# Kernel optimization log

Measured on AMD Instinct MI355X. Metric: run time of the kernel, lower is better.

## Reference

```python
import jax, jax.numpy as jnp
import numpy as np

SIGMA = 4.0
KSIZE = 2 * int(4.0 * SIGMA + 0.5) + 1  # 33, as in AnomalyMapGenerator
IMAGE_SIZE = (224, 224)


def _gaussian_kernel1d(ksize, sigma):
    x = jnp.arange(ksize, dtype=jnp.float32) - ksize // 2
    g = jnp.exp(-(x * x) / (2.0 * sigma * sigma))
    return g / jnp.sum(g)


def _gaussian_blur2d(x):
    # x: [B, 1, H, W]; kornia-style GaussianBlur2d with reflect padding
    g = _gaussian_kernel1d(KSIZE, SIGMA)
    k2 = jnp.outer(g, g)[None, None]  # [1,1,K,K]
    pad = KSIZE // 2
    xp = jnp.pad(x, ((0, 0), (0, 0), (pad, pad), (pad, pad)), mode='reflect')
    return jax.lax.conv_general_dilated(xp, k2, (1, 1), 'VALID')


def _cdist(a, b):
    # Euclidean distance matrix [Na, Nb] via the expanded quadratic form
    d2 = (jnp.sum(a * a, axis=1)[:, None]
          + jnp.sum(b * b, axis=1)[None, :]
          - 2.0 * (a @ b.T))
    return jnp.sqrt(jnp.maximum(d2, 1e-12))


def setup_inputs() -> dict:
    key = jax.random.key(0)
    k1, k2 = jax.random.split(key)
    B, H, W, C, M = 16, 28, 28, 128, 16384
    embedding = jax.random.normal(k1, (B * H * W, C), dtype=jnp.float32)
    memory_bank = jax.random.normal(k2, (M, C), dtype=jnp.float32)
    return {
        'embedding': embedding,
        'memory_bank': memory_bank,
        'batch_size': B,
        'width': W,
        'height': H,
        'num_neighbors': 9,
    }


def reference(embedding, memory_bank, batch_size, width, height, num_neighbors):
    N, C = embedding.shape
    # 1-NN search: [N, M] distance matrix
    dists = _cdist(embedding, memory_bank)
    locations_flat = jnp.argmin(dists, axis=1)                      # [N]
    patch_scores_flat = jnp.take_along_axis(
        dists, locations_flat[:, None], axis=1)[:, 0]                # [N]
    patch_scores = patch_scores_flat.reshape(batch_size, -1)        # [B, HW]
    locations = locations_flat.reshape(batch_size, -1)              # [B, HW]

    # compute_anomaly_score (softmax-reweighted max patch score)
    brange = jnp.arange(batch_size)
    max_patches = jnp.argmax(patch_scores, axis=1)                  # [B]
    score = patch_scores[brange, max_patches]                       # s* per image
    nn_index = locations[brange, max_patches]                       # [B]
    nn_sample = memory_bank[nn_index]                               # [B, C]
    d_nn = _cdist(nn_sample, memory_bank)                           # [B, M]
    _, support = jax.lax.top_k(-d_nn, num_neighbors)                # [B, k]
    max_feats = embedding.reshape(batch_size, -1, C)[brange, max_patches]  # [B, C]
    support_feats = memory_bank[support]                            # [B, k, C]
    d = jnp.sqrt(jnp.maximum(
        jnp.sum((max_feats[:, None, :] - support_feats) ** 2, axis=-1), 1e-12))  # [B, k]
    weights = 1.0 - jax.nn.softmax(d, axis=1)[:, 0]
    pred_score = weights * score                                    # [B]

    # anomaly map: nearest interpolate [B,1,w,h] -> IMAGE_SIZE, then blur
    pmap = patch_scores.reshape(batch_size, 1, width, height)
    rows = jnp.arange(IMAGE_SIZE[0]) * width // IMAGE_SIZE[0]
    cols = jnp.arange(IMAGE_SIZE[1]) * height // IMAGE_SIZE[1]
    up = pmap[:, :, rows][:, :, :, cols]                            # [B,1,224,224]
    anomaly_map = _gaussian_blur2d(up)
    return anomaly_map, pred_score
```

## Files before the change

### kernel.cpp

```cpp
#include <hip/hip_runtime.h>
#include <math.h>

#define C 128
#define BIAS 256.0f

typedef __attribute__((ext_vector_type(8))) short short8;
typedef __attribute__((ext_vector_type(4))) float f32x4;
typedef __attribute__((ext_vector_type(4))) unsigned int uint4v;
typedef unsigned short u16;
typedef unsigned int u32;
typedef unsigned long long u64;

static __device__ __forceinline__ u16 f2bf(float f) {
  unsigned int u = __builtin_bit_cast(unsigned int, f);
  unsigned int r = (u + 0x7fffu + ((u >> 16) & 1u)) >> 16;
  return (u16)r;
}

static __device__ __forceinline__ float bf2f(short s) {
  return __uint_as_float(((u32)(u16)s) << 16);
}

static __device__ __forceinline__ void gload_lds16(const void* g, void* l) {
  __builtin_amdgcn_global_load_lds(
      (const __attribute__((address_space(1))) unsigned int*)g,
      (__attribute__((address_space(3))) unsigned int*)l, 16, 0, 0);
}

__global__ __launch_bounds__(256) void prep_kernel(
    const float* __restrict__ emb, const float* __restrict__ bank,
    u16* __restrict__ Abf, u16* __restrict__ Bbf, float* __restrict__ anorm,
    float* __restrict__ bnorm, u64* __restrict__ packed, int N, int M) {
  const int tid = threadIdx.x;
  const int chunk = blockIdx.x * 256 + tid;
  const int total = (N + M) * (C / 8);
  if (chunk >= total) return;
  if (chunk < N) packed[chunk] = ~0ull;
  const int gr = chunk >> 4;
  const int co = (chunk & 15) * 8;
  const float* src;
  u16* dst;
  float* ndst;
  int r;
  float sc;
  if (gr < N) { src = emb; dst = Abf; ndst = anorm; r = gr; sc = 1.0f; }
  else { src = bank; dst = Bbf; ndst = bnorm; r = gr - N; sc = -2.0f; }
  const float* p = src + (size_t)r * C + co;
  float4 v0 = *(const float4*)p;
  float4 v1 = *(const float4*)(p + 4);
  u16 o[8] = {f2bf(sc * v0.x), f2bf(sc * v0.y), f2bf(sc * v0.z),
              f2bf(sc * v0.w), f2bf(sc * v1.x), f2bf(sc * v1.y),
              f2bf(sc * v1.z), f2bf(sc * v1.w)};
  *(uint4v*)(dst + (size_t)r * C + co) = *(const uint4v*)o;
  float s = v0.x * v0.x + v0.y * v0.y + v0.z * v0.z + v0.w * v0.w +
            v1.x * v1.x + v1.y * v1.y + v1.z * v1.z + v1.w * v1.w;
#pragma unroll
  for (int m = 1; m <= 8; m <<= 1) s += __shfl_xor(s, m, 64);
  if ((tid & 15) == 0) ndst[r] = s;
}

__global__ __launch_bounds__(256, 4) void nn_mfma(
    const u16* __restrict__ Abf, const u16* __restrict__ Bbf,
    const float* __restrict__ bnorm, const float* __restrict__ anorm,
    u64* __restrict__ packed, int N, int M) {
  __shared__ short Bs[2][8192];
  const int tid = threadIdx.x;
  const int lane = tid & 63;
  const int w = tid >> 6;
  const int lr = lane & 15, kg = lane >> 4;
  const int bid = blockIdx.x;
  const int sub = bid & 15;
  const int row0 = (bid >> 4) * 128;
  const int j0base = (sub & 7) * (M >> 3) + (sub >> 3) * (M >> 4);

  int soff[4];
#pragma unroll
  for (int q = 0; q < 4; ++q) {
    const int r = q * 16 + (tid >> 4);
    const int c = (((tid & 15) * 16) ^ ((r & 7) << 4)) >> 1;
    soff[q] = r * C + c;
  }

#define STAGE(bufi, jj)                                                     \
  do {                                                                      \
    const u16* gsrc = Bbf + (size_t)(jj) * C;                               \
    _Pragma("unroll") for (int q = 0; q < 4; ++q)                           \
        gload_lds16(gsrc + soff[q], &Bs[bufi][q * 2048 + w * 512]);         \
  } while (0)

  short8 af[2][4];
  {
    const u16* pa = Abf + (size_t)(row0 + w * 32 + lr) * C + kg * 8;
#pragma unroll
    for (int fi = 0; fi < 2; ++fi)
#pragma unroll
      for (int k = 0; k < 4; ++k)
        af[fi][k] = *(const short8*)(pa + fi * 16 * C + k * 32);
  }

  u32 minv[8];
#pragma unroll
  for (int s = 0; s < 8; ++s) minv[s] = 0xFFFFFFFFu;

  STAGE(0, j0base);

  const float* bnp = bnorm + j0base + lr;
  float bnc[4], bnn[4];
#pragma unroll
  for (int fj = 0; fj < 4; ++fj) bnc[fj] = bnp[fj * 16] + BIAS;

  __syncthreads();

  int j0 = j0base;
  for (int t = 0; t < 16; ++t) {
    const int buf = t & 1;
    if (t < 15) {
      STAGE(buf ^ 1, j0 + 64);
#pragma unroll
      for (int fj = 0; fj < 4; ++fj)
        bnn[fj] = bnp[(t + 1) * 64 + fj * 16] + BIAS;
    }

    f32x4 acc[2][4];
#pragma unroll
    for (int fi = 0; fi < 2; ++fi)
#pragma unroll
      for (int fj = 0; fj < 4; ++fj)
        acc[fi][fj] = (f32x4){bnc[fj], bnc[fj], bnc[fj], bnc[fj]};

    const short* bsb = &Bs[buf][0];
    const int cxor = (lr & 7) << 3;
#pragma unroll
    for (int k = 0; k < 4; ++k) {
      const int ko = (k * 32 + kg * 8) ^ cxor;
      short8 bf[4];
#pragma unroll
      for (int fj = 0; fj < 4; ++fj)
        bf[fj] = *(const short8*)&bsb[(fj * 16 + lr) * C + ko];
#pragma unroll
      for (int fi = 0; fi < 2; ++fi)
#pragma unroll
        for (int fj = 0; fj < 4; ++fj)
          acc[fi][fj] = __builtin_amdgcn_mfma_f32_16x16x32_bf16(
              af[fi][k], bf[fj], acc[fi][fj], 0, 0, 0);
    }

#pragma unroll
    for (int fj = 0; fj < 4; ++fj) {
      const u32 col = (u32)(j0 + fj * 16 + lr);
#pragma unroll
      for (int fi = 0; fi < 2; ++fi) {
#pragma unroll
        for (int r = 0; r < 4; ++r) {
          u32 key = (__float_as_uint(acc[fi][fj][r]) & 0xFFFFC000u) | col;
          const int s = fi * 4 + r;
          minv[s] = key < minv[s] ? key : minv[s];
        }
      }
    }
#pragma unroll
    for (int fj = 0; fj < 4; ++fj) bnc[fj] = bnn[fj];
    __syncthreads();
    j0 += 64;
  }
#undef STAGE

#pragma unroll
  for (int s = 0; s < 8; ++s) {
    u32 k = minv[s];
#pragma unroll
    for (int m = 1; m <= 8; m <<= 1) {
      u32 ok = (u32)__shfl_xor((int)k, m, 64);
      k = ok < k ? ok : k;
    }
    if (lr == 0) {
      const int row = row0 + w * 32 + (s >> 2) * 16 + kg * 4 + (s & 3);
      const u32 col = k & 0x3FFFu;
      const float vm = __uint_as_float(k & 0xFFFFC000u);
      float d2 = fmaxf(anorm[row] + (vm - BIAS), 0.0f);
      u64 pk = ((u64)__float_as_uint(d2) << 32) | col;
      atomicMin(&packed[row], pk);
    }
  }
}

__global__ __launch_bounds__(256) void rescore_part(
    const u16* __restrict__ Bbf, const float* __restrict__ bnorm,
    const u64* __restrict__ packed, float* __restrict__ score,
    int* __restrict__ maxrow, float* __restrict__ cvals,
    int* __restrict__ cidx, int M) {
  const int c = blockIdx.x;
  const int b = blockIdx.y;
  const int tid = threadIdx.x;
  __shared__ float vecf[C];
  __shared__ float sv[256];
  __shared__ int si[256];
  __shared__ int sl[256];

  {
    float bv = -INFINITY;
    int bi_ = 0x7fffffff, bl = 0;
    for (int i = tid; i < 784; i += 256) {
      u64 p = packed[(size_t)b * 784 + i];
      float v = __uint_as_float((unsigned)(p >> 32));
      if (v > bv) { bv = v; bi_ = i; bl = (int)(unsigned)p; }
    }
    sv[tid] = bv; si[tid] = bi_; sl[tid] = bl;
    __syncthreads();
    for (int s = 128; s > 0; s >>= 1) {
      if (tid < s) {
        if (sv[tid + s] > sv[tid] ||
            (sv[tid + s] == sv[tid] && si[tid + s] < si[tid])) {
          sv[tid] = sv[tid + s]; si[tid] = si[tid + s]; sl[tid] = sl[tid + s];
        }
      }
      __syncthreads();
    }
  }
  const int nn = sl[0];
  if (c == 0 && tid == 0) {
    score[b] = sqrtf(fmaxf(sv[0], 1e-12f));
    maxrow[b] = b * 784 + si[0];
  }
  __syncthreads();

  if (tid < 16) {
    short8 v = ((const short8*)(Bbf + (size_t)nn * C))[tid];
#pragma unroll
    for (int e = 0; e < 8; ++e) vecf[tid * 8 + e] = bf2f(v[e]);
  }
  __syncthreads();
  const float nnorm = bnorm[nn];
  const int j0 = c * (M >> 4);
  float rv[4];
  int rj[4];
#pragma unroll
  for (int q = 0; q < 4; ++q) {
    const int j = j0 + q * 256 + tid;
    const short8* br = (const short8*)(Bbf + (size_t)j * C);
    float dot = 0.0f;
#pragma unroll
    for (int kc = 0; kc < 16; ++kc) {
      short8 v = br[kc];
      float4 w0 = *(const float4*)&vecf[kc * 8];
      float4 w1 = *(const float4*)&vecf[kc * 8 + 4];
      dot += bf2f(v[0]) * w0.x + bf2f(v[1]) * w0.y + bf2f(v[2]) * w0.z +
             bf2f(v[3]) * w0.w + bf2f(v[4]) * w1.x + bf2f(v[5]) * w1.y +
             bf2f(v[6]) * w1.z + bf2f(v[7]) * w1.w;
    }
    rv[q] = nnorm + bnorm[j] - 0.5f * dot;
    rj[q] = j;
  }
  for (int s9 = 0; s9 < 9; ++s9) {
    float bv = INFINITY;
    int bj = 0x7fffffff;
#pragma unroll
    for (int q = 0; q < 4; ++q)
      if (rv[q] < bv) { bv = rv[q]; bj = rj[q]; }
    sv[tid] = bv; si[tid] = bj;
    __syncthreads();
    for (int s = 128; s > 0; s >>= 1) {
      if (tid < s) {
        if (sv[tid + s] < sv[tid] ||
            (sv[tid + s] == sv[tid] && si[tid + s] < si[tid])) {
          sv[tid] = sv[tid + s]; si[tid] = si[tid + s];
        }
      }
      __syncthreads();
    }
    const int selj = si[0];
    if (tid == 0) {
      cvals[((size_t)b * 16 + c) * 9 + s9] = sv[0];
      cidx[((size_t)b * 16 + c) * 9 + s9] = selj;
    }
#pragma unroll
    for (int q = 0; q < 4; ++q)
      if (rj[q] == selj) rv[q] = INFINITY;
    __syncthreads();
  }
}

__global__ __launch_bounds__(256) void rescore_merge(
    const float* __restrict__ emb, const float* __restrict__ Bk,
    const float* __restrict__ cvals, const int* __restrict__ cidx,
    const float* __restrict__ score, const int* __restrict__ maxrow,
    float* __restrict__ pred) {
  const int b = blockIdx.x;
  const int tid = threadIdx.x;
  const int w = tid >> 6, lane = tid & 63;
  __shared__ float wv[144];
  __shared__ int wi[144];
  __shared__ float sv[256];
  __shared__ int si[256];
  __shared__ int sp[256];
  __shared__ int sup[9];
  __shared__ float vec[C];
  __shared__ float ds[9];
  if (tid < 144) {
    wv[tid] = cvals[(size_t)b * 144 + tid];
    wi[tid] = cidx[(size_t)b * 144 + tid];
  }
  if (tid < 32)
    *(float4*)&vec[tid * 4] =
        *(const float4*)(emb + (size_t)maxrow[b] * C + tid * 4);
  __syncthreads();
  for (int s9 = 0; s9 < 9; ++s9) {
    if (tid < 144) { sv[tid] = wv[tid]; si[tid] = wi[tid]; sp[tid] = tid; }
    else { sv[tid] = INFINITY; si[tid] = 0x7fffffff; sp[tid] = -1; }
    __syncthreads();
    for (int s = 128; s > 0; s >>= 1) {
      if (tid < s) {
        if (sv[tid + s] < sv[tid] ||
            (sv[tid + s] == sv[tid] && si[tid + s] < si[tid])) {
          sv[tid] = sv[tid + s]; si[tid] = si[tid + s]; sp[tid] = sp[tid + s];
        }
      }
      __syncthreads();
    }
    if (tid == 0) {
      sup[s9] = si[0];
      wv[sp[0]] = INFINITY;
    }
    __syncthreads();
  }
  for (int s = w; s < 9; s += 4) {
    const float* br = Bk + (size_t)sup[s] * C;
    float d0 = vec[lane * 2] - br[lane * 2];
    float d1 = vec[lane * 2 + 1] - br[lane * 2 + 1];
    float acc = d0 * d0 + d1 * d1;
#pragma unroll
    for (int m = 1; m <= 32; m <<= 1) acc += __shfl_xor(acc, m, 64);
    if (lane == 0) ds[s] = sqrtf(fmaxf(acc, 1e-12f));
  }
  __syncthreads();
  if (tid == 0) {
    float m = ds[0];
    for (int t = 1; t < 9; ++t) m = fmaxf(m, ds[t]);
    float sum = 0.0f, e0 = 0.0f;
    for (int t = 0; t < 9; ++t) {
      float e = expf(ds[t] - m);
      sum += e;
      if (t == 0) e0 = e;
    }
    pred[b] = (1.0f - e0 / sum) * score[b];
  }
}

__global__ __launch_bounds__(256) void blur_fused(
    const u64* __restrict__ packed, float* __restrict__ out) {
  const int y = blockIdx.x, b = blockIdx.y;
  const int tid = threadIdx.x;
  __shared__ float g[33];
  __shared__ float rows[6][28];
  if (tid < 33) {
    float d = (float)tid - 16.0f;
    g[tid] = expf(-(d * d) * (1.0f / 32.0f));
  }
  int rcmin = 27;
  for (int t = 0; t < 33; ++t) {
    int yy = y + t - 16;
    yy = yy < 0 ? -yy : (yy > 223 ? 446 - yy : yy);
    int rc = yy >> 3;
    rcmin = rc < rcmin ? rc : rcmin;
  }
  if (tid < 168) {
    const int i = tid / 28, cc = tid - i * 28;
    int rc = rcmin + i;
    rc = rc > 27 ? 27 : rc;
    u64 p = packed[(size_t)b * 784 + rc * 28 + cc];
    float d2 = __uint_as_float((unsigned)(p >> 32));
    rows[i][cc] = sqrtf(fmaxf(d2, 1e-12f));
  }
  __syncthreads();
  float gv[6];
#pragma unroll
  for (int i = 0; i < 6; ++i) gv[i] = 0.0f;
  for (int t = 0; t < 33; ++t) {
    int yy = y + t - 16;
    yy = yy < 0 ? -yy : (yy > 223 ? 446 - yy : yy);
    const int idx = (yy >> 3) - rcmin;
    const float gt = g[t];
#pragma unroll
    for (int i = 0; i < 6; ++i) gv[i] += (idx == i) ? gt : 0.0f;
  }
  if (tid < 224) {
    float hacc[6];
#pragma unroll
    for (int i = 0; i < 6; ++i) hacc[i] = 0.0f;
    for (int s = 0; s < 33; ++s) {
      int xx = tid + s - 16;
      xx = xx < 0 ? -xx : (xx > 223 ? 446 - xx : xx);
      const int cs = xx >> 3;
      const float gs_ = g[s];
#pragma unroll
      for (int i = 0; i < 6; ++i) hacc[i] += gs_ * rows[i][cs];
    }
    float acc = 0.0f, gsum = 0.0f;
#pragma unroll
    for (int i = 0; i < 6; ++i) { acc += gv[i] * hacc[i]; gsum += gv[i]; }
    out[((size_t)b * 224 + y) * 224 + tid] = acc / (gsum * gsum);
  }
}

extern "C" void kernel_launch(void* const* d_in, const int* in_sizes, int n_in,
                              void* d_out, int out_size, void* d_ws,
                              size_t ws_size, hipStream_t stream) {
  const float* emb = (const float*)d_in[0];
  const float* bank = (const float*)d_in[1];
  const int N = in_sizes[0] / C;
  const int M = in_sizes[1] / C;
  const int B = 16;

  u16* Abf = (u16*)d_ws;
  u16* Bbf = Abf + (size_t)N * C;
  u64* packed = (u64*)(Bbf + (size_t)M * C);
  float* anorm = (float*)(packed + N);
  float* bnorm = anorm + N;
  float* score = bnorm + M;
  int* maxrow = (int*)(score + B);
  float* cvals = (float*)(maxrow + B);
  int* cidx = (int*)(cvals + B * 144);

  float* out_map = (float*)d_out;
  float* out_pred = out_map + (size_t)B * 224 * 224;

  const int total = (N + M) * (C / 8);
  prep_kernel<<<(total + 255) / 256, 256, 0, stream>>>(emb, bank, Abf, Bbf,
                                                       anorm, bnorm, packed,
                                                       N, M);
  nn_mfma<<<(N / 128) * 16, 256, 0, stream>>>(Abf, Bbf, bnorm, anorm, packed,
                                              N, M);
  blur_fused<<<dim3(224, B), 256, 0, stream>>>(packed, out_map);
  rescore_part<<<dim3(16, B), 256, 0, stream>>>(Bbf, bnorm, packed, score,
                                                maxrow, cvals, cidx, M);
  rescore_merge<<<B, 256, 0, stream>>>(emb, bank, cvals, cidx, score, maxrow,
                                       out_pred);
}
```

Before: 139.3 us.

## Fuse rescore merge via last-block atomic counter and batch blur rows per block

The separate rescore merge kernel is folded into the partial rescore kernel. A per-image atomic counter lets the last of 32 blocks perform the final top-9 merge and softmax weighting. The partial search is split across twice as many blocks, each covering half as many bank rows, to raise parallelism. The blur kernel now computes 8 output rows per block, sharing one horizontal pass over 5 source rows, and hoists the normalization into a single reciprocal. Together these aim to cut launch overhead and redundant horizontal blur work, at the cost of threadfence and atomic synchronization and more candidates in the merge.

```diff
diff --git a/kernel.cpp b/kernel.cpp
--- a/kernel.cpp
+++ b/kernel.cpp
@@ -30,12 +30,14 @@
 __global__ __launch_bounds__(256) void prep_kernel(
     const float* __restrict__ emb, const float* __restrict__ bank,
     u16* __restrict__ Abf, u16* __restrict__ Bbf, float* __restrict__ anorm,
-    float* __restrict__ bnorm, u64* __restrict__ packed, int N, int M) {
+    float* __restrict__ bnorm, u64* __restrict__ packed, int* __restrict__ cnt,
+    int N, int M) {
   const int tid = threadIdx.x;
   const int chunk = blockIdx.x * 256 + tid;
   const int total = (N + M) * (C / 8);
   if (chunk >= total) return;
   if (chunk < N) packed[chunk] = ~0ull;
+  if (chunk < 16) cnt[chunk] = 0;
   const int gr = chunk >> 4;
   const int co = (chunk & 15) * 8;
   const float* src;
@@ -184,11 +186,13 @@
   }
 }
 
-__global__ __launch_bounds__(256) void rescore_part(
+__global__ __launch_bounds__(256) void rescore_fused(
     const u16* __restrict__ Bbf, const float* __restrict__ bnorm,
-    const u64* __restrict__ packed, float* __restrict__ score,
+    const u64* __restrict__ packed, const float* __restrict__ emb,
+    const float* __restrict__ Bk, float* __restrict__ score,
     int* __restrict__ maxrow, float* __restrict__ cvals,
-    int* __restrict__ cidx, int M) {
+    int* __restrict__ cidx, int* __restrict__ cnt, float* __restrict__ pred,
+    int M) {
   const int c = blockIdx.x;
   const int b = blockIdx.y;
   const int tid = threadIdx.x;
@@ -196,6 +200,11 @@
   __shared__ float sv[256];
   __shared__ int si[256];
   __shared__ int sl[256];
+  __shared__ float wv[288];
+  __shared__ int wi[288];
+  __shared__ int sp[256];
+  __shared__ int sup[9];
+  __shared__ float ds[9];
 
   {
     float bv = -INFINITY;
@@ -231,11 +240,11 @@
   }
   __syncthreads();
   const float nnorm = bnorm[nn];
-  const int j0 = c * (M >> 4);
-  float rv[4];
-  int rj[4];
-#pragma unroll
-  for (int q = 0; q < 4; ++q) {
+  const int j0 = c * (M >> 5);
+  float rv[2];
+  int rj[2];
+#pragma unroll
+  for (int q = 0; q < 2; ++q) {
     const int j = j0 + q * 256 + tid;
     const short8* br = (const short8*)(Bbf + (size_t)j * C);
     float dot = 0.0f;
@@ -255,7 +264,7 @@
     float bv = INFINITY;
     int bj = 0x7fffffff;
 #pragma unroll
-    for (int q = 0; q < 4; ++q)
+    for (int q = 0; q < 2; ++q)
       if (rv[q] < bv) { bv = rv[q]; bj = rj[q]; }
     sv[tid] = bv; si[tid] = bj;
     __syncthreads();
@@ -270,43 +279,40 @@
     }
     const int selj = si[0];
     if (tid == 0) {
-      cvals[((size_t)b * 16 + c) * 9 + s9] = sv[0];
-      cidx[((size_t)b * 16 + c) * 9 + s9] = selj;
-    }
-#pragma unroll
-    for (int q = 0; q < 4; ++q)
+      cvals[((size_t)b * 32 + c) * 9 + s9] = sv[0];
+      cidx[((size_t)b * 32 + c) * 9 + s9] = selj;
+    }
+#pragma unroll
+    for (int q = 0; q < 2; ++q)
       if (rj[q] == selj) rv[q] = INFINITY;
     __syncthreads();
   }
-}
-
-__global__ __launch_bounds__(256) void rescore_merge(
-    const float* __restrict__ emb, const float* __restrict__ Bk,
-    const float* __restrict__ cvals, const int* __restrict__ cidx,
-    const float* __restrict__ score, const int* __restrict__ maxrow,
-    float* __restrict__ pred) {
-  const int b = blockIdx.x;
-  const int tid = threadIdx.x;
-  const int w = tid >> 6, lane = tid & 63;
-  __shared__ float wv[144];
-  __shared__ int wi[144];
-  __shared__ float sv[256];
-  __shared__ int si[256];
-  __shared__ int sp[256];
-  __shared__ int sup[9];
-  __shared__ float vec[C];
-  __shared__ float ds[9];
-  if (tid < 144) {
-    wv[tid] = cvals[(size_t)b * 144 + tid];
-    wi[tid] = cidx[(size_t)b * 144 + tid];
+
+  if (tid == 0) {
+    __threadfence();
+    sl[0] = atomicAdd(&cnt[b], 1);
+  }
+  __syncthreads();
+  if (sl[0] != 31) return;
+  __threadfence();
+
+  for (int i = tid; i < 288; i += 256) {
+    wv[i] = cvals[(size_t)b * 288 + i];
+    wi[i] = cidx[(size_t)b * 288 + i];
   }
   if (tid < 32)
-    *(float4*)&vec[tid * 4] =
+    *(float4*)&vecf[tid * 4] =
         *(const float4*)(emb + (size_t)maxrow[b] * C + tid * 4);
   __syncthreads();
   for (int s9 = 0; s9 < 9; ++s9) {
-    if (tid < 144) { sv[tid] = wv[tid]; si[tid] = wi[tid]; sp[tid] = tid; }
-    else { sv[tid] = INFINITY; si[tid] = 0x7fffffff; sp[tid] = -1; }
+    float bv = INFINITY;
+    int bi_ = 0x7fffffff, bp = -1;
+    for (int i = tid; i < 288; i += 256) {
+      if (wv[i] < bv || (wv[i] == bv && wi[i] < bi_)) {
+        bv = wv[i]; bi_ = wi[i]; bp = i;
+      }
+    }
+    sv[tid] = bv; si[tid] = bi_; sp[tid] = bp;
     __syncthreads();
     for (int s = 128; s > 0; s >>= 1) {
       if (tid < s) {
@@ -323,10 +329,11 @@
     }
     __syncthreads();
   }
+  const int w = tid >> 6, lane = tid & 63;
   for (int s = w; s < 9; s += 4) {
     const float* br = Bk + (size_t)sup[s] * C;
-    float d0 = vec[lane * 2] - br[lane * 2];
-    float d1 = vec[lane * 2 + 1] - br[lane * 2 + 1];
+    float d0 = vecf[lane * 2] - br[lane * 2];
+    float d1 = vecf[lane * 2 + 1] - br[lane * 2 + 1];
     float acc = d0 * d0 + d1 * d1;
 #pragma unroll
     for (int m = 1; m <= 32; m <<= 1) acc += __shfl_xor(acc, m, 64);
@@ -348,57 +355,60 @@
 
 __global__ __launch_bounds__(256) void blur_fused(
     const u64* __restrict__ packed, float* __restrict__ out) {
-  const int y = blockIdx.x, b = blockIdx.y;
+  const int q = blockIdx.x, b = blockIdx.y;
   const int tid = threadIdx.x;
   __shared__ float g[33];
-  __shared__ float rows[6][28];
+  __shared__ float rows[5][28];
+  __shared__ float gvs[8][5];
+  __shared__ float ginv;
+  const int rc0 = q < 2 ? 0 : (q > 25 ? 23 : q - 2);
   if (tid < 33) {
     float d = (float)tid - 16.0f;
     g[tid] = expf(-(d * d) * (1.0f / 32.0f));
   }
-  int rcmin = 27;
-  for (int t = 0; t < 33; ++t) {
-    int yy = y + t - 16;
-    yy = yy < 0 ? -yy : (yy > 223 ? 446 - yy : yy);
-    int rc = yy >> 3;
-    rcmin = rc < rcmin ? rc : rcmin;
-  }
-  if (tid < 168) {
+  if (tid < 140) {
     const int i = tid / 28, cc = tid - i * 28;
-    int rc = rcmin + i;
-    rc = rc > 27 ? 27 : rc;
-    u64 p = packed[(size_t)b * 784 + rc * 28 + cc];
+    u64 p = packed[(size_t)b * 784 + (rc0 + i) * 28 + cc];
     float d2 = __uint_as_float((unsigned)(p >> 32));
     rows[i][cc] = sqrtf(fmaxf(d2, 1e-12f));
   }
   __syncthreads();
-  float gv[6];
-#pragma unroll
-  for (int i = 0; i < 6; ++i) gv[i] = 0.0f;
-  for (int t = 0; t < 33; ++t) {
-    int yy = y + t - 16;
-    yy = yy < 0 ? -yy : (yy > 223 ? 446 - yy : yy);
-    const int idx = (yy >> 3) - rcmin;
-    const float gt = g[t];
-#pragma unroll
-    for (int i = 0; i < 6; ++i) gv[i] += (idx == i) ? gt : 0.0f;
-  }
+  if (tid == 0) {
+    float s = 0.0f;
+    for (int t = 0; t < 33; ++t) s += g[t];
+    ginv = 1.0f / (s * s);
+  }
+  if (tid < 40) {
+    const int dy = tid / 5, i = tid - dy * 5;
+    const int y = q * 8 + dy;
+    float acc = 0.0f;
+    for (int t = 0; t < 33; ++t) {
+      int yy = y + t - 16;
+      yy = yy < 0 ? -yy : (yy > 223 ? 446 - yy : yy);
+      acc += ((yy >> 3) - rc0 == i) ? g[t] : 0.0f;
+    }
+    gvs[dy][i] = acc;
+  }
+  __syncthreads();
   if (tid < 224) {
-    float hacc[6];
-#pragma unroll
-    for (int i = 0; i < 6; ++i) hacc[i] = 0.0f;
+    float hacc[5];
+#pragma unroll
+    for (int i = 0; i < 5; ++i) hacc[i] = 0.0f;
     for (int s = 0; s < 33; ++s) {
       int xx = tid + s - 16;
       xx = xx < 0 ? -xx : (xx > 223 ? 446 - xx : xx);
       const int cs = xx >> 3;
       const float gs_ = g[s];
 #pragma unroll
-      for (int i = 0; i < 6; ++i) hacc[i] += gs_ * rows[i][cs];
-    }
-    float acc = 0.0f, gsum = 0.0f;
-#pragma unroll
-    for (int i = 0; i < 6; ++i) { acc += gv[i] * hacc[i]; gsum += gv[i]; }
-    out[((size_t)b * 224 + y) * 224 + tid] = acc / (gsum * gsum);
+      for (int i = 0; i < 5; ++i) hacc[i] += gs_ * rows[i][cs];
+    }
+#pragma unroll
+    for (int dy = 0; dy < 8; ++dy) {
+      float acc = 0.0f;
+#pragma unroll
+      for (int i = 0; i < 5; ++i) acc += gvs[dy][i] * hacc[i];
+      out[((size_t)b * 224 + q * 8 + dy) * 224 + tid] = acc * ginv;
+    }
   }
 }
 
@@ -419,20 +429,19 @@
   float* score = bnorm + M;
   int* maxrow = (int*)(score + B);
   float* cvals = (float*)(maxrow + B);
-  int* cidx = (int*)(cvals + B * 144);
+  int* cidx = (int*)(cvals + B * 288);
+  int* cnt = cidx + B * 288;
 
   float* out_map = (float*)d_out;
   float* out_pred = out_map + (size_t)B * 224 * 224;
 
   const int total = (N + M) * (C / 8);
-  prep_kernel<<<(total + 255) / 256, 256, 0, stream>>>(emb, bank, Abf, Bbf,
-                                                       anorm, bnorm, packed,
-                                                       N, M);
+  prep_kernel<<<(total + 255) / 256, 256, 0, stream>>>(
+      emb, bank, Abf, Bbf, anorm, bnorm, packed, cnt, N, M);
   nn_mfma<<<(N / 128) * 16, 256, 0, stream>>>(Abf, Bbf, bnorm, anorm, packed,
                                               N, M);
-  blur_fused<<<dim3(224, B), 256, 0, stream>>>(packed, out_map);
-  rescore_part<<<dim3(16, B), 256, 0, stream>>>(Bbf, bnorm, packed, score,
-                                                maxrow, cvals, cidx, M);
-  rescore_merge<<<B, 256, 0, stream>>>(emb, bank, cvals, cidx, score, maxrow,
-                                       out_pred);
-}
+  blur_fused<<<dim3(28, B), 256, 0, stream>>>(packed, out_map);
+  rescore_fused<<<dim3(32, B), 256, 0, stream>>>(Bbf, bnorm, packed, emb, bank,
+                                                 score, maxrow, cvals, cidx,
+                                                 cnt, out_pred, M);
+}
```

Result: faster. 128.4 us (-7.8%).
